# Optimization experiments

Hardware: AMD Instinct MI355X
Metric: run time of the kernel (lower is better)

## Reference

```python
import jax, jax.numpy as jnp
import numpy as np

DIM_PROBLEM = 8192
DIM_CONTEXT = 512
DIM_HIDDEN = 1024


def setup_inputs() -> dict:
    key = jax.random.key(0)
    ks = jax.random.split(key, 8)
    s = 0.02
    H, C = DIM_HIDDEN, DIM_CONTEXT
    return {
        "context": jax.random.normal(ks[0], (C,), jnp.float32),
        # linear_1: dim_context -> 1
        "W1": jax.random.normal(ks[1], (1, C), jnp.float32) * s,
        "b1": jnp.zeros((1,), jnp.float32),
        # LSTM layer 0 (input dim 1), torch gate order [i, f, g, o]
        "Wih0": jax.random.normal(ks[2], (4 * H, 1), jnp.float32) * s,
        "Whh0": jax.random.normal(ks[3], (4 * H, H), jnp.float32) * s,
        "bih0": jnp.zeros((4 * H,), jnp.float32),
        "bhh0": jnp.zeros((4 * H,), jnp.float32),
        # LSTM layer 1 (input dim H)
        "Wih1": jax.random.normal(ks[4], (4 * H, H), jnp.float32) * s,
        "Whh1": jax.random.normal(ks[5], (4 * H, H), jnp.float32) * s,
        "bih1": jnp.zeros((4 * H,), jnp.float32),
        "bhh1": jnp.zeros((4 * H,), jnp.float32),
        # linear_2: dim_hidden -> 1
        "W2": jax.random.normal(ks[6], (1, H), jnp.float32) * s,
        "b2": jnp.zeros((1,), jnp.float32),
    }


def _lstm_cell(gin, h, c, Whh, b):
    # gin = W_ih @ x (precomputed); torch gate order i, f, g, o
    gates = gin + Whh @ h + b
    i, f, g, o = jnp.split(gates, 4)
    i, f, o = jax.nn.sigmoid(i), jax.nn.sigmoid(f), jax.nn.sigmoid(o)
    g = jnp.tanh(g)
    c = f * c + i * g
    return o * jnp.tanh(c), c


def reference(context, W1, b1, Wih0, Whh0, bih0, bhh0, Wih1, Whh1, bih1, bhh1, W2, b2):
    H = Whh0.shape[1]
    x0 = (W1 @ context + b1)[0]  # linear_1 seeds the first LSTM input (scalar)
    b0 = bih0 + bhh0
    b1g = bih1 + bhh1
    keys = jax.random.split(jax.random.key(42), DIM_PROBLEM)

    def step(carry, k):
        h0, c0, h1, c1, x, logp = carry
        h0, c0 = _lstm_cell(Wih0[:, 0] * x, h0, c0, Whh0, b0)
        h1, c1 = _lstm_cell(Wih1 @ h0, h1, c1, Whh1, b1g)
        p = jax.nn.sigmoid(W2 @ h1 + b2)[0]
        # Bernoulli sample; detached as in the original (.clone().detach(), .item())
        s = jax.lax.stop_gradient(jax.random.bernoulli(k, p).astype(jnp.float32))
        # log of running product  p^s * (1-p)^(1-s)
        logp = logp + s * jnp.log(p) + (1.0 - s) * jnp.log1p(-p)
        return (h0, c0, h1, c1, s, logp), s

    z = jnp.zeros((H,), jnp.float32)
    carry0 = (z, z, z, z, x0, jnp.float32(0.0))
    (_, _, _, _, _, logp), solution = jax.lax.scan(step, carry0, keys)
    return solution, logp
```

## Files before the change

kernel.cpp:

```cpp
#include <hip/hip_runtime.h>
#include <stdint.h>
#include <math.h>


#define H     1024
#define NSTEP 8192
#define NWG   512
#define BLK   64
#define NROW  25

typedef _Float16 h2 __attribute__((ext_vector_type(2)));
typedef _Float16 h8 __attribute__((ext_vector_type(8)));
typedef unsigned long long u64;

union U32H2 { uint32_t u; h2 v; };

__device__ __forceinline__ u64 pack2(float v0, float v1, uint32_t tag){
  U32H2 p; p.v.x = (_Float16)v0; p.v.y = (_Float16)v1;
  return ((u64)tag << 32) | (u64)p.u;
}

__device__ __forceinline__ uint2 tf2x32(uint32_t k0, uint32_t k1, uint32_t x0, uint32_t x1){
  uint32_t k2 = k0 ^ k1 ^ 0x1BD11BDAu;
  x0 += k0; x1 += k1;
#define TFR(r) { x0 += x1; x1 = (x1 << (r)) | (x1 >> (32 - (r))); x1 ^= x0; }
  TFR(13) TFR(15) TFR(26) TFR(6)
  x0 += k1; x1 += k2 + 1u;
  TFR(17) TFR(29) TFR(16) TFR(24)
  x0 += k2; x1 += k0 + 2u;
  TFR(13) TFR(15) TFR(26) TFR(6)
  x0 += k0; x1 += k1 + 3u;
  TFR(17) TFR(29) TFR(16) TFR(24)
  x0 += k1; x1 += k2 + 4u;
  TFR(13) TFR(15) TFR(26) TFR(6)
  x0 += k2; x1 += k0 + 5u;
#undef TFR
  uint2 r; r.x = x0; r.y = x1; return r;
}

__device__ __forceinline__ uint32_t jax_word(uint32_t i){
  return (i < 8192u) ? tf2x32(0u, 42u, i, i + 8192u).x
                     : tf2x32(0u, 42u, i - 8192u, i).y;
}

__device__ __forceinline__ float wred64(float x){
  #pragma unroll
  for(int off = 32; off > 0; off >>= 1) x += __shfl_xor(x, off, 64);
  return x;
}

__device__ __forceinline__ void mreduce8(int lane, const float* v, float* s){
  const bool b1 = lane & 1;
  float t, w0, w1, w2, w3;
  t = b1 ? v[0] : v[1]; w0 = (b1 ? v[1] : v[0]) + __shfl_xor(t, 1, 64);
  t = b1 ? v[2] : v[3]; w1 = (b1 ? v[3] : v[2]) + __shfl_xor(t, 1, 64);
  t = b1 ? v[4] : v[5]; w2 = (b1 ? v[5] : v[4]) + __shfl_xor(t, 1, 64);
  t = b1 ? v[6] : v[7]; w3 = (b1 ? v[7] : v[6]) + __shfl_xor(t, 1, 64);
  const bool b2 = lane & 2;
  float u0, u1;
  t = b2 ? w0 : w1; u0 = (b2 ? w1 : w0) + __shfl_xor(t, 2, 64);
  t = b2 ? w2 : w3; u1 = (b2 ? w3 : w2) + __shfl_xor(t, 2, 64);
  const bool b4 = lane & 4;
  t = b4 ? u0 : u1; float z = (b4 ? u1 : u0) + __shfl_xor(t, 4, 64);
  z += __shfl_xor(z, 8, 64);
  z += __shfl_xor(z, 16, 64);
  z += __shfl_xor(z, 32, 64);
  #pragma unroll
  for(int r = 0; r < 8; r++) s[r] = __shfl(z, r, 64);
}

#if __has_builtin(__builtin_amdgcn_fdot2)
__device__ __forceinline__ float fdot2f(h2 a, h2 b, float c){ return __builtin_amdgcn_fdot2(a, b, c, false); }
#else
__device__ __forceinline__ float fdot2f(h2 a, h2 b, float c){
  return (float)a.x * (float)b.x + (float)a.y * (float)b.y + c;
}
#endif

__device__ __forceinline__ float sigm(float x){
  x = fminf(fmaxf(x, -30.f), 30.f);
  return 1.f / (1.f + __expf(-x));
}
__device__ __forceinline__ float tanh_f(float x){
  x = fminf(fmaxf(x, -15.f), 15.f);
  float e = __expf(2.f * x);
  return (e - 1.f) / (e + 1.f);
}

__device__ __forceinline__ u64 ld_slot(const u64* p){
  return __hip_atomic_load((u64*)p, __ATOMIC_RELAXED, __HIP_MEMORY_SCOPE_AGENT);
}
__device__ __forceinline__ void st_slot(u64* p, u64 v){
  __hip_atomic_store(p, v, __ATOMIC_RELAXED, __HIP_MEMORY_SCOPE_AGENT);
}

__device__ __forceinline__ void poll_h(const u64* __restrict__ buf,
                                       uint32_t tag, int lane, h2* hv){
  const u64* p0 = buf + (lane << 2);
  const u64* p1 = buf + 256 + (lane << 2);
  u64 pv[8];
  #pragma unroll
  for(int k = 0; k < 4; k++) pv[k]     = ld_slot(p0 + k);
  #pragma unroll
  for(int k = 0; k < 4; k++) pv[4 + k] = ld_slot(p1 + k);
  for(;;){
    uint32_t bad = 0;
    #pragma unroll
    for(int k = 0; k < 8; k++) bad |= ((uint32_t)(pv[k] >> 32)) ^ tag;
    if(!bad) break;
    __builtin_amdgcn_s_sleep(1);
    #pragma unroll
    for(int k = 0; k < 4; k++) if(((uint32_t)(pv[k] >> 32)) != tag)   pv[k]     = ld_slot(p0 + k);
    #pragma unroll
    for(int k = 0; k < 4; k++) if(((uint32_t)(pv[4+k] >> 32)) != tag) pv[4+k]   = ld_slot(p1 + k);
  }
  #pragma unroll
  for(int k = 0; k < 8; k++){ U32H2 p; p.u = (uint32_t)pv[k]; hv[k] = p.v; }
}

__device__ __forceinline__ void publish(u64* __restrict__ rep, int wg, int lane, u64 pk){
  if(lane < 8) st_slot(rep + (lane << 9) + wg, pk);
}

__device__ __forceinline__ float row_part(const h2* __restrict__ wrow, int lane, const h2* hv){
  h8 wl = *(const h8*)(wrow + (lane << 2));
  h8 wh = *(const h8*)(wrow + 256 + (lane << 2));
  float a0 = 0.f, a1 = 0.f;
  h2 w;
  w = __builtin_shufflevector(wl, wl, 0, 1); a0 = fdot2f(w, hv[0], a0);
  w = __builtin_shufflevector(wl, wl, 2, 3); a1 = fdot2f(w, hv[1], a1);
  w = __builtin_shufflevector(wl, wl, 4, 5); a0 = fdot2f(w, hv[2], a0);
  w = __builtin_shufflevector(wl, wl, 6, 7); a1 = fdot2f(w, hv[3], a1);
  w = __builtin_shufflevector(wh, wh, 0, 1); a0 = fdot2f(w, hv[4], a0);
  w = __builtin_shufflevector(wh, wh, 2, 3); a1 = fdot2f(w, hv[5], a1);
  w = __builtin_shufflevector(wh, wh, 4, 5); a0 = fdot2f(w, hv[6], a0);
  w = __builtin_shufflevector(wh, wh, 6, 7); a1 = fdot2f(w, hv[7], a1);
  return a0 + a1;
}

__global__ void __launch_bounds__(BLK)
lstm_persist(const float* __restrict__ ctx,  const float* __restrict__ W1p,  const float* __restrict__ b1p,
             const float* __restrict__ Wih0, const float* __restrict__ Whh0,
             const float* __restrict__ bih0, const float* __restrict__ bhh0,
             const float* __restrict__ Wih1, const float* __restrict__ Whh1,
             const float* __restrict__ bih1, const float* __restrict__ bhh1,
             const float* __restrict__ W2p,  const float* __restrict__ b2p,
             float* __restrict__ out,
             u64* __restrict__ h0rep,
             u64* __restrict__ h1rep)
{
  __shared__ h2 w[NROW][H/2];

  const int lane = threadIdx.x;
  const int wg   = blockIdx.x;
  const int j0   = wg << 1;
  const u64* myh0 = h0rep + ((size_t)(wg & 7) << 9);
  const u64* myh1 = h1rep + ((size_t)(wg & 7) << 9);

  #pragma unroll 1
  for(int r = 0; r < NROW; r++){
    const float* rowp;
    if(r < 8)      { int g = r & 3,  j = j0 + (r >> 2);                   rowp = Wih1 + (size_t)(g*H + j)*H; }
    else if(r < 16){ int rr = r - 8;  int g = rr & 3, j = j0 + (rr >> 2); rowp = Whh0 + (size_t)(g*H + j)*H; }
    else if(r < 24){ int rr = r - 16; int g = rr & 3, j = j0 + (rr >> 2); rowp = Whh1 + (size_t)(g*H + j)*H; }
    else           rowp = W2p;
    const float4* s4 = (const float4*)rowp;
    #pragma unroll
    for(int it = 0; it < 4; it++){
      float4 f = s4[lane + (it << 6)];
      h2 pa; pa.x = (_Float16)f.x; pa.y = (_Float16)f.y;
      h2 pb; pb.x = (_Float16)f.z; pb.y = (_Float16)f.w;
      const int ci = (lane + (it << 6)) << 1;
      w[r][ci] = pa; w[r][ci + 1] = pb;
    }
  }
  __syncthreads();

  float b0g[8], b1g[8], w0g[8];
  #pragma unroll
  for(int e = 0; e < 2; e++){
    const int j = j0 + e;
    #pragma unroll
    for(int g = 0; g < 4; g++){
      b0g[4*e + g] = bih0[g*H + j] + bhh0[g*H + j];
      b1g[4*e + g] = bih1[g*H + j] + bhh1[g*H + j];
      w0g[4*e + g] = Wih0[g*H + j];
    }
  }
  const float b2v = b2p[0];

  float xacc = 0.f;
  for(int c = lane; c < 512; c += 64) xacc += W1p[c] * ctx[c];
  const float x0 = wred64(xacc) + b1p[0];

  float c0v[2], c1v[2] = {0.f, 0.f}, logp = 0.f;
  float a1[8] = {0.f,0.f,0.f,0.f,0.f,0.f,0.f,0.f};
  float ubatch = 0.f;

  {
    float h00[2];
    #pragma unroll
    for(int e = 0; e < 2; e++){
      float gi = sigm (w0g[4*e+0]*x0 + b0g[4*e+0]);
      float gg = tanh_f(w0g[4*e+2]*x0 + b0g[4*e+2]);
      float go = sigm (w0g[4*e+3]*x0 + b0g[4*e+3]);
      c0v[e] = gi * gg;
      h00[e] = go * tanh_f(c0v[e]);
    }
    publish(h0rep, wg, lane, pack2(h00[0], h00[1], 1u));
  }

  h2 hv[8];

  #pragma unroll 1
  for(int t = 0; t < NSTEP; t++){
    const uint32_t tt = (uint32_t)t;

    poll_h(myh0, tt + 1u, lane, hv);

    float pr[8], s1[8];
    #pragma unroll
    for(int r = 0; r < 8; r++) pr[r] = row_part(&w[r][0], lane, hv);
    mreduce8(lane, pr, s1);
    {
      float h1v[2];
      #pragma unroll
      for(int e = 0; e < 2; e++){
        float gi = sigm (s1[4*e+0] + a1[4*e+0] + b1g[4*e+0]);
        float gf = sigm (s1[4*e+1] + a1[4*e+1] + b1g[4*e+1]);
        float gg = tanh_f(s1[4*e+2] + a1[4*e+2] + b1g[4*e+2]);
        float go = sigm (s1[4*e+3] + a1[4*e+3] + b1g[4*e+3]);
        c1v[e] = gf*c1v[e] + gi*gg;
        h1v[e] = go * tanh_f(c1v[e]);
      }
      publish(h1rep, wg, lane, pack2(h1v[0], h1v[1], tt + 1u));
    }

    if((t & 63) == 0){
      const uint32_t i0 = (uint32_t)t + (uint32_t)lane;
      const uint32_t kk0 = jax_word(2u*i0), kk1 = jax_word(2u*i0 + 1u);
      const uint32_t bits = tf2x32(kk0, kk1, 0u, 0u).x;
      ubatch = __uint_as_float((bits >> 9) | 0x3f800000u) - 1.0f;
    }
    float a0p[8], a0[8];
    #pragma unroll
    for(int r = 0; r < 8; r++) a0p[r] = row_part(&w[8 + r][0], lane, hv);
    mreduce8(lane, a0p, a0);

    float c0c[2][2], h0c[2][2];
    #pragma unroll
    for(int e = 0; e < 2; e++){
      #pragma unroll
      for(int sb = 0; sb < 2; sb++){
        const float sv = (float)sb;
        float gi = sigm (a0[4*e+0] + w0g[4*e+0]*sv + b0g[4*e+0]);
        float gf = sigm (a0[4*e+1] + w0g[4*e+1]*sv + b0g[4*e+1]);
        float gg = tanh_f(a0[4*e+2] + w0g[4*e+2]*sv + b0g[4*e+2]);
        float go = sigm (a0[4*e+3] + w0g[4*e+3]*sv + b0g[4*e+3]);
        float cc = gf*c0v[e] + gi*gg;
        c0c[e][sb] = cc;
        h0c[e][sb] = go * tanh_f(cc);
      }
    }

    poll_h(myh1, tt + 1u, lane, hv);

    float z = row_part(&w[24][0], lane, hv);
    z = wred64(z) + b2v;
    const float p = sigm(z);
    const float u = __shfl(ubatch, t & 63, 64);
    const bool  sb_ = (u < p);
    c0v[0] = sb_ ? c0c[0][1] : c0c[0][0];
    c0v[1] = sb_ ? c0c[1][1] : c0c[1][0];
    publish(h0rep, wg, lane,
            pack2(sb_ ? h0c[0][1] : h0c[0][0], sb_ ? h0c[1][1] : h0c[1][0], tt + 2u));

    logp += sb_ ? __logf(p) : __logf(1.f - p);
    if(wg == 0 && lane == 0) out[t] = sb_ ? 1.f : 0.f;

    float a1p[8];
    #pragma unroll
    for(int r = 0; r < 8; r++) a1p[r] = row_part(&w[16 + r][0], lane, hv);
    mreduce8(lane, a1p, a1);
  }

  if(wg == 0 && lane == 0) out[NSTEP] = logp;
}

extern "C" void kernel_launch(void* const* d_in, const int* in_sizes, int n_in,
                              void* d_out, int out_size, void* d_ws, size_t ws_size,
                              hipStream_t stream){
  u64* h0rep = (u64*)d_ws;
  u64* h1rep = h0rep + 8 * 512;
  hipLaunchKernelGGL(lstm_persist, dim3(NWG), dim3(BLK), 0, stream,
    (const float*)d_in[0],  (const float*)d_in[1],  (const float*)d_in[2],
    (const float*)d_in[3],  (const float*)d_in[4],  (const float*)d_in[5],  (const float*)d_in[6],
    (const float*)d_in[7],  (const float*)d_in[8],  (const float*)d_in[9],  (const float*)d_in[10],
    (const float*)d_in[11], (const float*)d_in[12],
    (float*)d_out, h0rep, h1rep);
}
```

Measured before the change: 36.67 ms.

## Add dedicated poller wavefront staging hidden states into LDS, drop replicated buffers

Each workgroup grows to two wavefronts. The second wave busy-polls the global h0/h1 exchange buffers and stages the values into double-buffered LDS, handing them over through workgroup-scope flags. The compute wave waits only on the LDS flags. The 8-way replicated publish buffers are replaced by a single copy written by one lane, so all 512 workgroups now poll the same 512 slots. This aims to take global polling latency off the compute wave's critical path and cut publish stores, at the cost of more contention on the shared slots, extra LDS handshakes, and an extra wave per CU.

```diff
diff --git a/kernel.cpp b/kernel.cpp
--- a/kernel.cpp
+++ b/kernel.cpp
@@ -6,7 +6,7 @@
 #define H     1024
 #define NSTEP 8192
 #define NWG   512
-#define BLK   64
+#define BLK   128
 #define NROW  25
 
 typedef _Float16 h2 __attribute__((ext_vector_type(2)));
@@ -94,8 +94,8 @@
   __hip_atomic_store(p, v, __ATOMIC_RELAXED, __HIP_MEMORY_SCOPE_AGENT);
 }
 
-__device__ __forceinline__ void poll_h(const u64* __restrict__ buf,
-                                       uint32_t tag, int lane, h2* hv){
+__device__ __forceinline__ void stage_poll(const u64* __restrict__ buf, uint32_t tag,
+                                           uint32_t* __restrict__ dst, int lane){
   const u64* p0 = buf + (lane << 2);
   const u64* p1 = buf + 256 + (lane << 2);
   u64 pv[8];
@@ -108,18 +108,25 @@
     #pragma unroll
     for(int k = 0; k < 8; k++) bad |= ((uint32_t)(pv[k] >> 32)) ^ tag;
     if(!bad) break;
-    __builtin_amdgcn_s_sleep(1);
-    #pragma unroll
-    for(int k = 0; k < 4; k++) if(((uint32_t)(pv[k] >> 32)) != tag)   pv[k]     = ld_slot(p0 + k);
-    #pragma unroll
-    for(int k = 0; k < 4; k++) if(((uint32_t)(pv[4+k] >> 32)) != tag) pv[4+k]   = ld_slot(p1 + k);
+    #pragma unroll
+    for(int k = 0; k < 4; k++) if(((uint32_t)(pv[k] >> 32)) != tag)   pv[k]   = ld_slot(p0 + k);
+    #pragma unroll
+    for(int k = 0; k < 4; k++) if(((uint32_t)(pv[4+k] >> 32)) != tag) pv[4+k] = ld_slot(p1 + k);
   }
-  #pragma unroll
-  for(int k = 0; k < 8; k++){ U32H2 p; p.u = (uint32_t)pv[k]; hv[k] = p.v; }
-}
-
-__device__ __forceinline__ void publish(u64* __restrict__ rep, int wg, int lane, u64 pk){
-  if(lane < 8) st_slot(rep + (lane << 9) + wg, pk);
+  uint4 a; a.x = (uint32_t)pv[0]; a.y = (uint32_t)pv[1]; a.z = (uint32_t)pv[2]; a.w = (uint32_t)pv[3];
+  uint4 b; b.x = (uint32_t)pv[4]; b.y = (uint32_t)pv[5]; b.z = (uint32_t)pv[6]; b.w = (uint32_t)pv[7];
+  *(uint4*)(dst + (lane << 2))       = a;
+  *(uint4*)(dst + 256 + (lane << 2)) = b;
+}
+
+__device__ __forceinline__ void ld_hv(const uint32_t* __restrict__ src, int lane, h2* hv){
+  uint4 a = *(const uint4*)(src + (lane << 2));
+  uint4 b = *(const uint4*)(src + 256 + (lane << 2));
+  U32H2 p;
+  p.u = a.x; hv[0] = p.v;  p.u = a.y; hv[1] = p.v;
+  p.u = a.z; hv[2] = p.v;  p.u = a.w; hv[3] = p.v;
+  p.u = b.x; hv[4] = p.v;  p.u = b.y; hv[5] = p.v;
+  p.u = b.z; hv[6] = p.v;  p.u = b.w; hv[7] = p.v;
 }
 
 __device__ __forceinline__ float row_part(const h2* __restrict__ wrow, int lane, const h2* hv){
@@ -146,16 +153,21 @@
              const float* __restrict__ bih1, const float* __restrict__ bhh1,
              const float* __restrict__ W2p,  const float* __restrict__ b2p,
              float* __restrict__ out,
-             u64* __restrict__ h0rep,
-             u64* __restrict__ h1rep)
+             u64* __restrict__ h0buf,
+             u64* __restrict__ h1buf)
 {
   __shared__ h2 w[NROW][H/2];
-
-  const int lane = threadIdx.x;
+  __shared__ uint32_t stg[2][2][H/2];
+  __shared__ int flg[2][2];
+  __shared__ int done[2];
+
+  const int tid  = threadIdx.x;
+  const int wv   = tid >> 6;
+  const int lane = tid & 63;
   const int wg   = blockIdx.x;
   const int j0   = wg << 1;
-  const u64* myh0 = h0rep + ((size_t)(wg & 7) << 9);
-  const u64* myh1 = h1rep + ((size_t)(wg & 7) << 9);
+
+  if(tid == 0){ flg[0][0] = flg[0][1] = flg[1][0] = flg[1][1] = 0; done[0] = done[1] = 0; }
 
   #pragma unroll 1
   for(int r = 0; r < NROW; r++){
@@ -166,136 +178,162 @@
     else           rowp = W2p;
     const float4* s4 = (const float4*)rowp;
     #pragma unroll
-    for(int it = 0; it < 4; it++){
-      float4 f = s4[lane + (it << 6)];
+    for(int it = 0; it < 2; it++){
+      float4 f = s4[tid + (it << 7)];
       h2 pa; pa.x = (_Float16)f.x; pa.y = (_Float16)f.y;
       h2 pb; pb.x = (_Float16)f.z; pb.y = (_Float16)f.w;
-      const int ci = (lane + (it << 6)) << 1;
+      const int ci = (tid + (it << 7)) << 1;
       w[r][ci] = pa; w[r][ci + 1] = pb;
     }
   }
   __syncthreads();
 
-  float b0g[8], b1g[8], w0g[8];
-  #pragma unroll
-  for(int e = 0; e < 2; e++){
-    const int j = j0 + e;
-    #pragma unroll
-    for(int g = 0; g < 4; g++){
-      b0g[4*e + g] = bih0[g*H + j] + bhh0[g*H + j];
-      b1g[4*e + g] = bih1[g*H + j] + bhh1[g*H + j];
-      w0g[4*e + g] = Wih0[g*H + j];
-    }
+  if(wv == 1){
+    #pragma unroll 1
+    for(int t = 0; t < NSTEP; t++){
+      const int want = t + 1;
+      const int p = want & 1;
+      while(__hip_atomic_load(&done[0], __ATOMIC_ACQUIRE, __HIP_MEMORY_SCOPE_WORKGROUP) < want - 2)
+        __builtin_amdgcn_s_sleep(1);
+      stage_poll(h0buf, (uint32_t)want, &stg[0][p][0], lane);
+      __hip_atomic_store(&flg[0][p], want, __ATOMIC_RELEASE, __HIP_MEMORY_SCOPE_WORKGROUP);
+
+      while(__hip_atomic_load(&done[1], __ATOMIC_ACQUIRE, __HIP_MEMORY_SCOPE_WORKGROUP) < want - 2)
+        __builtin_amdgcn_s_sleep(1);
+      stage_poll(h1buf, (uint32_t)want, &stg[1][p][0], lane);
+      __hip_atomic_store(&flg[1][p], want, __ATOMIC_RELEASE, __HIP_MEMORY_SCOPE_WORKGROUP);
+    }
+  } else {
+    float b0g[8], b1g[8], w0g[8];
+    #pragma unroll
+    for(int e = 0; e < 2; e++){
+      const int j = j0 + e;
+      #pragma unroll
+      for(int g = 0; g < 4; g++){
+        b0g[4*e + g] = bih0[g*H + j] + bhh0[g*H + j];
+        b1g[4*e + g] = bih1[g*H + j] + bhh1[g*H + j];
+        w0g[4*e + g] = Wih0[g*H + j];
+      }
+    }
+    const float b2v = b2p[0];
+
+    float xacc = 0.f;
+    for(int c = lane; c < 512; c += 64) xacc += W1p[c] * ctx[c];
+    const float x0 = wred64(xacc) + b1p[0];
+
+    float c0v[2], c1v[2] = {0.f, 0.f}, logp = 0.f;
+    float a1[8] = {0.f,0.f,0.f,0.f,0.f,0.f,0.f,0.f};
+    float ubatch = 0.f;
+
+    {
+      float h00[2];
+      #pragma unroll
+      for(int e = 0; e < 2; e++){
+        float gi = sigm (w0g[4*e+0]*x0 + b0g[4*e+0]);
+        float gg = tanh_f(w0g[4*e+2]*x0 + b0g[4*e+2]);
+        float go = sigm (w0g[4*e+3]*x0 + b0g[4*e+3]);
+        c0v[e] = gi * gg;
+        h00[e] = go * tanh_f(c0v[e]);
+      }
+      if(lane == 0) st_slot(&h0buf[wg], pack2(h00[0], h00[1], 1u));
+    }
+
+    h2 hv[8];
+
+    #pragma unroll 1
+    for(int t = 0; t < NSTEP; t++){
+      const uint32_t tt = (uint32_t)t;
+      const int want = t + 1;
+      const int p = want & 1;
+
+      while(__hip_atomic_load(&flg[0][p], __ATOMIC_ACQUIRE, __HIP_MEMORY_SCOPE_WORKGROUP) != want)
+        __builtin_amdgcn_s_sleep(1);
+      ld_hv(&stg[0][p][0], lane, hv);
+      __hip_atomic_store(&done[0], want, __ATOMIC_RELEASE, __HIP_MEMORY_SCOPE_WORKGROUP);
+
+      float pr[8], s1[8];
+      #pragma unroll
+      for(int r = 0; r < 8; r++) pr[r] = row_part(&w[r][0], lane, hv);
+      mreduce8(lane, pr, s1);
+      {
+        float h1v[2];
+        #pragma unroll
+        for(int e = 0; e < 2; e++){
+          float gi = sigm (s1[4*e+0] + a1[4*e+0] + b1g[4*e+0]);
+          float gf = sigm (s1[4*e+1] + a1[4*e+1] + b1g[4*e+1]);
+          float gg = tanh_f(s1[4*e+2] + a1[4*e+2] + b1g[4*e+2]);
+          float go = sigm (s1[4*e+3] + a1[4*e+3] + b1g[4*e+3]);
+          c1v[e] = gf*c1v[e] + gi*gg;
+          h1v[e] = go * tanh_f(c1v[e]);
+        }
+        if(lane == 0) st_slot(&h1buf[wg], pack2(h1v[0], h1v[1], (uint32_t)want));
+      }
+
+      if((t & 63) == 0){
+        const uint32_t i0 = (uint32_t)t + (uint32_t)lane;
+        const uint32_t kk0 = jax_word(2u*i0), kk1 = jax_word(2u*i0 + 1u);
+        const uint32_t bits = tf2x32(kk0, kk1, 0u, 0u).x;
+        ubatch = __uint_as_float((bits >> 9) | 0x3f800000u) - 1.0f;
+      }
+      float a0p[8], a0[8];
+      #pragma unroll
+      for(int r = 0; r < 8; r++) a0p[r] = row_part(&w[8 + r][0], lane, hv);
+      mreduce8(lane, a0p, a0);
+
+      float c0c[2][2], h0c[2][2];
+      #pragma unroll
+      for(int e = 0; e < 2; e++){
+        #pragma unroll
+        for(int sb = 0; sb < 2; sb++){
+          const float sv = (float)sb;
+          float gi = sigm (a0[4*e+0] + w0g[4*e+0]*sv + b0g[4*e+0]);
+          float gf = sigm (a0[4*e+1] + w0g[4*e+1]*sv + b0g[4*e+1]);
+          float gg = tanh_f(a0[4*e+2] + w0g[4*e+2]*sv + b0g[4*e+2]);
+          float go = sigm (a0[4*e+3] + w0g[4*e+3]*sv + b0g[4*e+3]);
+          float cc = gf*c0v[e] + gi*gg;
+          c0c[e][sb] = cc;
+          h0c[e][sb] = go * tanh_f(cc);
+        }
+      }
+
+      while(__hip_atomic_load(&flg[1][p], __ATOMIC_ACQUIRE, __HIP_MEMORY_SCOPE_WORKGROUP) != want)
+        __builtin_amdgcn_s_sleep(1);
+      ld_hv(&stg[1][p][0], lane, hv);
+      __hip_atomic_store(&done[1], want, __ATOMIC_RELEASE, __HIP_MEMORY_SCOPE_WORKGROUP);
+
+      float z = row_part(&w[24][0], lane, hv);
+      z = wred64(z) + b2v;
+      const float pp = sigm(z);
+      const float u = __shfl(ubatch, t & 63, 64);
+      const bool  sb_ = (u < pp);
+      c0v[0] = sb_ ? c0c[0][1] : c0c[0][0];
+      c0v[1] = sb_ ? c0c[1][1] : c0c[1][0];
+      if(lane == 0)
+        st_slot(&h0buf[wg], pack2(sb_ ? h0c[0][1] : h0c[0][0],
+                                  sb_ ? h0c[1][1] : h0c[1][0], tt + 2u));
+
+      logp += sb_ ? __logf(pp) : __logf(1.f - pp);
+      if(wg == 0 && lane == 0) out[t] = sb_ ? 1.f : 0.f;
+
+      float a1p[8];
+      #pragma unroll
+      for(int r = 0; r < 8; r++) a1p[r] = row_part(&w[16 + r][0], lane, hv);
+      mreduce8(lane, a1p, a1);
+    }
+
+    if(wg == 0 && lane == 0) out[NSTEP] = logp;
   }
-  const float b2v = b2p[0];
-
-  float xacc = 0.f;
-  for(int c = lane; c < 512; c += 64) xacc += W1p[c] * ctx[c];
-  const float x0 = wred64(xacc) + b1p[0];
-
-  float c0v[2], c1v[2] = {0.f, 0.f}, logp = 0.f;
-  float a1[8] = {0.f,0.f,0.f,0.f,0.f,0.f,0.f,0.f};
-  float ubatch = 0.f;
-
-  {
-    float h00[2];
-    #pragma unroll
-    for(int e = 0; e < 2; e++){
-      float gi = sigm (w0g[4*e+0]*x0 + b0g[4*e+0]);
-      float gg = tanh_f(w0g[4*e+2]*x0 + b0g[4*e+2]);
-      float go = sigm (w0g[4*e+3]*x0 + b0g[4*e+3]);
-      c0v[e] = gi * gg;
-      h00[e] = go * tanh_f(c0v[e]);
-    }
-    publish(h0rep, wg, lane, pack2(h00[0], h00[1], 1u));
-  }
-
-  h2 hv[8];
-
-  #pragma unroll 1
-  for(int t = 0; t < NSTEP; t++){
-    const uint32_t tt = (uint32_t)t;
-
-    poll_h(myh0, tt + 1u, lane, hv);
-
-    float pr[8], s1[8];
-    #pragma unroll
-    for(int r = 0; r < 8; r++) pr[r] = row_part(&w[r][0], lane, hv);
-    mreduce8(lane, pr, s1);
-    {
-      float h1v[2];
-      #pragma unroll
-      for(int e = 0; e < 2; e++){
-        float gi = sigm (s1[4*e+0] + a1[4*e+0] + b1g[4*e+0]);
-        float gf = sigm (s1[4*e+1] + a1[4*e+1] + b1g[4*e+1]);
-        float gg = tanh_f(s1[4*e+2] + a1[4*e+2] + b1g[4*e+2]);
-        float go = sigm (s1[4*e+3] + a1[4*e+3] + b1g[4*e+3]);
-        c1v[e] = gf*c1v[e] + gi*gg;
-        h1v[e] = go * tanh_f(c1v[e]);
-      }
-      publish(h1rep, wg, lane, pack2(h1v[0], h1v[1], tt + 1u));
-    }
-
-    if((t & 63) == 0){
-      const uint32_t i0 = (uint32_t)t + (uint32_t)lane;
-      const uint32_t kk0 = jax_word(2u*i0), kk1 = jax_word(2u*i0 + 1u);
-      const uint32_t bits = tf2x32(kk0, kk1, 0u, 0u).x;
-      ubatch = __uint_as_float((bits >> 9) | 0x3f800000u) - 1.0f;
-    }
-    float a0p[8], a0[8];
-    #pragma unroll
-    for(int r = 0; r < 8; r++) a0p[r] = row_part(&w[8 + r][0], lane, hv);
-    mreduce8(lane, a0p, a0);
-
-    float c0c[2][2], h0c[2][2];
-    #pragma unroll
-    for(int e = 0; e < 2; e++){
-      #pragma unroll
-      for(int sb = 0; sb < 2; sb++){
-        const float sv = (float)sb;
-        float gi = sigm (a0[4*e+0] + w0g[4*e+0]*sv + b0g[4*e+0]);
-        float gf = sigm (a0[4*e+1] + w0g[4*e+1]*sv + b0g[4*e+1]);
-        float gg = tanh_f(a0[4*e+2] + w0g[4*e+2]*sv + b0g[4*e+2]);
-        float go = sigm (a0[4*e+3] + w0g[4*e+3]*sv + b0g[4*e+3]);
-        float cc = gf*c0v[e] + gi*gg;
-        c0c[e][sb] = cc;
-        h0c[e][sb] = go * tanh_f(cc);
-      }
-    }
-
-    poll_h(myh1, tt + 1u, lane, hv);
-
-    float z = row_part(&w[24][0], lane, hv);
-    z = wred64(z) + b2v;
-    const float p = sigm(z);
-    const float u = __shfl(ubatch, t & 63, 64);
-    const bool  sb_ = (u < p);
-    c0v[0] = sb_ ? c0c[0][1] : c0c[0][0];
-    c0v[1] = sb_ ? c0c[1][1] : c0c[1][0];
-    publish(h0rep, wg, lane,
-            pack2(sb_ ? h0c[0][1] : h0c[0][0], sb_ ? h0c[1][1] : h0c[1][0], tt + 2u));
-
-    logp += sb_ ? __logf(p) : __logf(1.f - p);
-    if(wg == 0 && lane == 0) out[t] = sb_ ? 1.f : 0.f;
-
-    float a1p[8];
-    #pragma unroll
-    for(int r = 0; r < 8; r++) a1p[r] = row_part(&w[16 + r][0], lane, hv);
-    mreduce8(lane, a1p, a1);
-  }
-
-  if(wg == 0 && lane == 0) out[NSTEP] = logp;
 }
 
 extern "C" void kernel_launch(void* const* d_in, const int* in_sizes, int n_in,
                               void* d_out, int out_size, void* d_ws, size_t ws_size,
                               hipStream_t stream){
-  u64* h0rep = (u64*)d_ws;
-  u64* h1rep = h0rep + 8 * 512;
+  u64* h0buf = (u64*)d_ws;
+  u64* h1buf = h0buf + 512;
   hipLaunchKernelGGL(lstm_persist, dim3(NWG), dim3(BLK), 0, stream,
     (const float*)d_in[0],  (const float*)d_in[1],  (const float*)d_in[2],
     (const float*)d_in[3],  (const float*)d_in[4],  (const float*)d_in[5],  (const float*)d_in[6],
     (const float*)d_in[7],  (const float*)d_in[8],  (const float*)d_in[9],  (const float*)d_in[10],
     (const float*)d_in[11], (const float*)d_in[12],
-    (float*)d_out, h0rep, h1rep);
-}
+    (float*)d_out, h0buf, h1buf);
+}
```

After: 93.01 ms. 154% more time.

## Merge two per-step grid exchanges into one packed exchange with deferred sampling

Applied to the files above, without the earlier changes.

Restructures the persistent LSTM loop so each workgroup publishes both candidate h0 values (for sample 0 and 1) together with h1 in a single packed 64-bit slot, tagged with a 16-bit step counter in double-buffered storage. Every workgroup then recomputes p itself after a single poll and picks the right h0 candidate locally. This halves the number of cross-workgroup synchronisation points per timestep. The exchanged data grows because each lane now polls 16 slots instead of 8, the 8-way replicated buffers are dropped in favour of one shared buffer, and there is one extra loop iteration to finish the last sample. The 16-bit tag and the two-buffer scheme rely on the slots holding stale tags at launch, so results depend on how the workspace is initialised.

```diff
diff --git a/kernel.cpp b/kernel.cpp
--- a/kernel.cpp
+++ b/kernel.cpp
@@ -14,10 +14,12 @@
 typedef unsigned long long u64;
 
 union U32H2 { uint32_t u; h2 v; };
-
-__device__ __forceinline__ u64 pack2(float v0, float v1, uint32_t tag){
-  U32H2 p; p.v.x = (_Float16)v0; p.v.y = (_Float16)v1;
-  return ((u64)tag << 32) | (u64)p.u;
+union F16U  { _Float16 h; uint16_t u; };
+
+__device__ __forceinline__ uint32_t f16b(float x){ F16U f; f.h = (_Float16)x; return (uint32_t)f.u; }
+
+__device__ __forceinline__ u64 pack3(float c0c_, float c1c_, float h1_, uint32_t tag){
+  return (u64)(f16b(c0c_) | (f16b(c1c_) << 16)) | ((u64)(f16b(h1_) | (tag << 16)) << 32);
 }
 
 __device__ __forceinline__ uint2 tf2x32(uint32_t k0, uint32_t k1, uint32_t x0, uint32_t x1){
@@ -94,32 +96,41 @@
   __hip_atomic_store(p, v, __ATOMIC_RELAXED, __HIP_MEMORY_SCOPE_AGENT);
 }
 
-__device__ __forceinline__ void poll_h(const u64* __restrict__ buf,
-                                       uint32_t tag, int lane, h2* hv){
-  const u64* p0 = buf + (lane << 2);
-  const u64* p1 = buf + 256 + (lane << 2);
-  u64 pv[8];
-  #pragma unroll
-  for(int k = 0; k < 4; k++) pv[k]     = ld_slot(p0 + k);
-  #pragma unroll
-  for(int k = 0; k < 4; k++) pv[4 + k] = ld_slot(p1 + k);
+__device__ __forceinline__ void poll16(const u64* __restrict__ buf, uint32_t tag,
+                                       int lane, u64* pv){
+  const u64* p0 = buf + (lane << 3);
+  const u64* p1 = buf + 512 + (lane << 3);
+  #pragma unroll
+  for(int k = 0; k < 8; k++) pv[k]     = ld_slot(p0 + k);
+  #pragma unroll
+  for(int k = 0; k < 8; k++) pv[8 + k] = ld_slot(p1 + k);
   for(;;){
     uint32_t bad = 0;
     #pragma unroll
-    for(int k = 0; k < 8; k++) bad |= ((uint32_t)(pv[k] >> 32)) ^ tag;
+    for(int k = 0; k < 16; k++) bad |= ((uint32_t)(pv[k] >> 48)) ^ tag;
     if(!bad) break;
     __builtin_amdgcn_s_sleep(1);
     #pragma unroll
-    for(int k = 0; k < 4; k++) if(((uint32_t)(pv[k] >> 32)) != tag)   pv[k]     = ld_slot(p0 + k);
-    #pragma unroll
-    for(int k = 0; k < 4; k++) if(((uint32_t)(pv[4+k] >> 32)) != tag) pv[4+k]   = ld_slot(p1 + k);
-  }
-  #pragma unroll
-  for(int k = 0; k < 8; k++){ U32H2 p; p.u = (uint32_t)pv[k]; hv[k] = p.v; }
-}
-
-__device__ __forceinline__ void publish(u64* __restrict__ rep, int wg, int lane, u64 pk){
-  if(lane < 8) st_slot(rep + (lane << 9) + wg, pk);
+    for(int k = 0; k < 8; k++) if(((uint32_t)(pv[k] >> 48)) != tag)   pv[k]   = ld_slot(p0 + k);
+    #pragma unroll
+    for(int k = 0; k < 8; k++) if(((uint32_t)(pv[8+k] >> 48)) != tag) pv[8+k] = ld_slot(p1 + k);
+  }
+}
+
+__device__ __forceinline__ void extract(const u64* pv, h2* f_c0, h2* f_c1, h2* f_h1){
+  #pragma unroll
+  for(int g = 0; g < 2; g++){
+    #pragma unroll
+    for(int m = 0; m < 4; m++){
+      const u64 a = pv[8*g + 2*m], b = pv[8*g + 2*m + 1];
+      const uint32_t lo_a = (uint32_t)a, lo_b = (uint32_t)b;
+      const uint32_t hi_a = (uint32_t)(a >> 32), hi_b = (uint32_t)(b >> 32);
+      U32H2 p;
+      p.u = (lo_a & 0xffffu) | (lo_b << 16);        f_c0[4*g + m] = p.v;
+      p.u = (lo_a >> 16) | (lo_b & 0xffff0000u);    f_c1[4*g + m] = p.v;
+      p.u = (hi_a & 0xffffu) | (hi_b << 16);        f_h1[4*g + m] = p.v;
+    }
+  }
 }
 
 __device__ __forceinline__ float row_part(const h2* __restrict__ wrow, int lane, const h2* hv){
@@ -146,16 +157,13 @@
              const float* __restrict__ bih1, const float* __restrict__ bhh1,
              const float* __restrict__ W2p,  const float* __restrict__ b2p,
              float* __restrict__ out,
-             u64* __restrict__ h0rep,
-             u64* __restrict__ h1rep)
+             u64* __restrict__ sbuf)
 {
   __shared__ h2 w[NROW][H/2];
 
   const int lane = threadIdx.x;
   const int wg   = blockIdx.x;
   const int j0   = wg << 1;
-  const u64* myh0 = h0rep + ((size_t)(wg & 7) << 9);
-  const u64* myh1 = h1rep + ((size_t)(wg & 7) << 9);
 
   #pragma unroll 1
   for(int r = 0; r < NROW; r++){
@@ -194,108 +202,118 @@
   const float x0 = wred64(xacc) + b1p[0];
 
   float c0v[2], c1v[2] = {0.f, 0.f}, logp = 0.f;
-  float a1[8] = {0.f,0.f,0.f,0.f,0.f,0.f,0.f,0.f};
-  float ubatch = 0.f;
+  float c0c[2][2];
+  float ubatch = 1.f;
 
   {
-    float h00[2];
+    u64 pk[2];
     #pragma unroll
     for(int e = 0; e < 2; e++){
       float gi = sigm (w0g[4*e+0]*x0 + b0g[4*e+0]);
       float gg = tanh_f(w0g[4*e+2]*x0 + b0g[4*e+2]);
       float go = sigm (w0g[4*e+3]*x0 + b0g[4*e+3]);
-      c0v[e] = gi * gg;
-      h00[e] = go * tanh_f(c0v[e]);
-    }
-    publish(h0rep, wg, lane, pack2(h00[0], h00[1], 1u));
-  }
-
-  h2 hv[8];
+      float cc = gi * gg;
+      c0c[e][0] = c0c[e][1] = cc;
+      float h00 = go * tanh_f(cc);
+      pk[e] = pack3(h00, h00, 0.f, 0u);
+    }
+    if(lane < 2) st_slot(&sbuf[j0 + lane], pk[lane]);
+  }
 
   #pragma unroll 1
-  for(int t = 0; t < NSTEP; t++){
-    const uint32_t tt = (uint32_t)t;
-
-    poll_h(myh0, tt + 1u, lane, hv);
-
-    float pr[8], s1[8];
-    #pragma unroll
-    for(int r = 0; r < 8; r++) pr[r] = row_part(&w[r][0], lane, hv);
-    mreduce8(lane, pr, s1);
-    {
-      float h1v[2];
-      #pragma unroll
-      for(int e = 0; e < 2; e++){
-        float gi = sigm (s1[4*e+0] + a1[4*e+0] + b1g[4*e+0]);
-        float gf = sigm (s1[4*e+1] + a1[4*e+1] + b1g[4*e+1]);
-        float gg = tanh_f(s1[4*e+2] + a1[4*e+2] + b1g[4*e+2]);
-        float go = sigm (s1[4*e+3] + a1[4*e+3] + b1g[4*e+3]);
-        c1v[e] = gf*c1v[e] + gi*gg;
-        h1v[e] = go * tanh_f(c1v[e]);
-      }
-      publish(h1rep, wg, lane, pack2(h1v[0], h1v[1], tt + 1u));
-    }
-
-    if((t & 63) == 0){
-      const uint32_t i0 = (uint32_t)t + (uint32_t)lane;
+  for(int t = 0; t <= NSTEP; t++){
+    const uint32_t tag = (uint32_t)t & 0xffffu;
+    const u64* rbuf = sbuf + ((t & 1) << 10);
+
+    u64 pv[16];
+    poll16(rbuf, tag, lane, pv);
+    h2 f_c0[8], f_c1[8], f_h1[8];
+    extract(pv, f_c0, f_c1, f_h1);
+
+    float z = row_part(&w[24][0], lane, f_h1);
+    z = wred64(z) + b2v;
+    const float p = sigm(z);
+    const int idx = t - 1;
+    if(t >= 1 && (idx & 63) == 0){
+      const uint32_t i0 = (uint32_t)idx + (uint32_t)lane;
       const uint32_t kk0 = jax_word(2u*i0), kk1 = jax_word(2u*i0 + 1u);
       const uint32_t bits = tf2x32(kk0, kk1, 0u, 0u).x;
       ubatch = __uint_as_float((bits >> 9) | 0x3f800000u) - 1.0f;
     }
+    const float u = (t >= 1) ? __shfl(ubatch, idx & 63, 64) : 1.f;
+    const bool  sb_ = (u < p);
+
+    if(t == NSTEP){
+      logp += sb_ ? __logf(p) : __logf(1.f - p);
+      if(wg == 0 && lane == 0){ out[NSTEP - 1] = sb_ ? 1.f : 0.f; out[NSTEP] = logp; }
+      break;
+    }
+
+    h2 hv0[8];
+    #pragma unroll
+    for(int k = 0; k < 8; k++) hv0[k] = sb_ ? f_c1[k] : f_c0[k];
+    c0v[0] = sb_ ? c0c[0][1] : c0c[0][0];
+    c0v[1] = sb_ ? c0c[1][1] : c0c[1][0];
+
+    float pr[8], s1[8];
+    #pragma unroll
+    for(int r = 0; r < 8; r++)
+      pr[r] = row_part(&w[r][0], lane, hv0) + row_part(&w[16 + r][0], lane, f_h1);
+    mreduce8(lane, pr, s1);
+    float h1v[2];
+    #pragma unroll
+    for(int e = 0; e < 2; e++){
+      float gi = sigm (s1[4*e+0] + b1g[4*e+0]);
+      float gf = sigm (s1[4*e+1] + b1g[4*e+1]);
+      float gg = tanh_f(s1[4*e+2] + b1g[4*e+2]);
+      float go = sigm (s1[4*e+3] + b1g[4*e+3]);
+      c1v[e] = gf*c1v[e] + gi*gg;
+      h1v[e] = go * tanh_f(c1v[e]);
+    }
+
     float a0p[8], a0[8];
     #pragma unroll
-    for(int r = 0; r < 8; r++) a0p[r] = row_part(&w[8 + r][0], lane, hv);
+    for(int r = 0; r < 8; r++) a0p[r] = row_part(&w[8 + r][0], lane, hv0);
     mreduce8(lane, a0p, a0);
 
-    float c0c[2][2], h0c[2][2];
+    float h0c[2][2];
     #pragma unroll
     for(int e = 0; e < 2; e++){
       #pragma unroll
-      for(int sb = 0; sb < 2; sb++){
-        const float sv = (float)sb;
+      for(int sb2 = 0; sb2 < 2; sb2++){
+        const float sv = (float)sb2;
         float gi = sigm (a0[4*e+0] + w0g[4*e+0]*sv + b0g[4*e+0]);
         float gf = sigm (a0[4*e+1] + w0g[4*e+1]*sv + b0g[4*e+1]);
         float gg = tanh_f(a0[4*e+2] + w0g[4*e+2]*sv + b0g[4*e+2]);
         float go = sigm (a0[4*e+3] + w0g[4*e+3]*sv + b0g[4*e+3]);
         float cc = gf*c0v[e] + gi*gg;
-        c0c[e][sb] = cc;
-        h0c[e][sb] = go * tanh_f(cc);
+        c0c[e][sb2] = cc;
+        h0c[e][sb2] = go * tanh_f(cc);
       }
     }
 
-    poll_h(myh1, tt + 1u, lane, hv);
-
-    float z = row_part(&w[24][0], lane, hv);
-    z = wred64(z) + b2v;
-    const float p = sigm(z);
-    const float u = __shfl(ubatch, t & 63, 64);
-    const bool  sb_ = (u < p);
-    c0v[0] = sb_ ? c0c[0][1] : c0c[0][0];
-    c0v[1] = sb_ ? c0c[1][1] : c0c[1][0];
-    publish(h0rep, wg, lane,
-            pack2(sb_ ? h0c[0][1] : h0c[0][0], sb_ ? h0c[1][1] : h0c[1][0], tt + 2u));
-
-    logp += sb_ ? __logf(p) : __logf(1.f - p);
-    if(wg == 0 && lane == 0) out[t] = sb_ ? 1.f : 0.f;
-
-    float a1p[8];
-    #pragma unroll
-    for(int r = 0; r < 8; r++) a1p[r] = row_part(&w[16 + r][0], lane, hv);
-    mreduce8(lane, a1p, a1);
-  }
-
-  if(wg == 0 && lane == 0) out[NSTEP] = logp;
+    {
+      u64* wbuf = sbuf + (((t + 1) & 1) << 10);
+      u64 pk0 = pack3(h0c[0][0], h0c[0][1], h1v[0], (uint32_t)(t + 1) & 0xffffu);
+      u64 pk1 = pack3(h0c[1][0], h0c[1][1], h1v[1], (uint32_t)(t + 1) & 0xffffu);
+      if(lane < 2) st_slot(&wbuf[j0 + lane], lane ? pk1 : pk0);
+    }
+
+    if(t >= 1){
+      logp += sb_ ? __logf(p) : __logf(1.f - p);
+      if(wg == 0 && lane == 0) out[t - 1] = sb_ ? 1.f : 0.f;
+    }
+  }
 }
 
 extern "C" void kernel_launch(void* const* d_in, const int* in_sizes, int n_in,
                               void* d_out, int out_size, void* d_ws, size_t ws_size,
                               hipStream_t stream){
-  u64* h0rep = (u64*)d_ws;
-  u64* h1rep = h0rep + 8 * 512;
+  u64* sbuf = (u64*)d_ws;
   hipLaunchKernelGGL(lstm_persist, dim3(NWG), dim3(BLK), 0, stream,
     (const float*)d_in[0],  (const float*)d_in[1],  (const float*)d_in[2],
     (const float*)d_in[3],  (const float*)d_in[4],  (const float*)d_in[5],  (const float*)d_in[6],
     (const float*)d_in[7],  (const float*)d_in[8],  (const float*)d_in[9],  (const float*)d_in[10],
     (const float*)d_in[11], (const float*)d_in[12],
-    (float*)d_out, h0rep, h1rep);
-}
+    (float*)d_out, sbuf);
+}
```

Measured after the change: 65.61 ms. 1.79x slower.
